# Kernel tuning notes

Hardware: AMD Instinct MI355X
Metric: run time of the kernel (lower is better)

The kernel has to match this reference:

```python
import jax, jax.numpy as jnp
import numpy as np
from jax import lax

B, N = 16, 131072
NUM_CLASSES = 2
OUTPUT_BOX_NUM = 500
IOU_THRESHOLD = 0.3
SCORE_THRESHOLD = 0.7
NEG = jnp.float32(-1e30)
DELTA_SCALE = jnp.array([0.1, 0.2], dtype=jnp.float32)


def setup_inputs() -> dict:
    key = jax.random.key(0)
    k1, k2, k3, k4, k5, k6 = jax.random.split(key, 6)
    deltas = jax.random.normal(k1, (B, N, 2), dtype=jnp.float32)
    class_logits = jax.random.normal(k2, (B, N, NUM_CLASSES), dtype=jnp.float32)
    # CTPN-style anchors: fixed-width 16px columns, varying y-center / height
    cy = jax.random.uniform(k3, (B, N), dtype=jnp.float32) * 1024.0
    h = 8.0 + jax.random.uniform(k4, (B, N), dtype=jnp.float32) * 56.0
    col = jax.random.randint(k5, (B, N), 0, 64).astype(jnp.float32) * 16.0
    anchors = jnp.stack([cy - 0.5 * h, col, cy + 0.5 * h, col + 16.0], axis=-1)  # [B,N,4] (y1,x1,y2,x2)
    valid_anchors_indices = jax.random.randint(k6, (B, N), 0, N)
    return {
        'deltas': deltas,
        'class_logits': class_logits,
        'anchors': anchors,
        'valid_anchors_indices': valid_anchors_indices,
    }


def apply_regress(deltas, anchors):
    # deltas [N,2] (dy,dh); anchors [N,4] (y1,x1,y2,x2)
    h = anchors[:, 2] - anchors[:, 0]
    cy = (anchors[:, 2] + anchors[:, 0]) * 0.5
    d = deltas * DELTA_SCALE
    cy = cy + d[:, 0] * h
    h = h * jnp.exp(d[:, 1])
    return jnp.stack([cy - 0.5 * h, anchors[:, 1], cy + 0.5 * h, anchors[:, 3]], axis=1)


def iou_one_to_many(box, boxes):
    yy1 = jnp.maximum(box[0], boxes[:, 0])
    xx1 = jnp.maximum(box[1], boxes[:, 1])
    yy2 = jnp.minimum(box[2], boxes[:, 2])
    xx2 = jnp.minimum(box[3], boxes[:, 3])
    inter = jnp.maximum(yy2 - yy1, 0.0) * jnp.maximum(xx2 - xx1, 0.0)
    a1 = (box[2] - box[0]) * (box[3] - box[1])
    a2 = (boxes[:, 2] - boxes[:, 0]) * (boxes[:, 3] - boxes[:, 1])
    return inter / (a1 + a2 - inter + 1e-8)


def nms_indices(boxes, scores):
    # Greedy NMS, fixed OUTPUT_BOX_NUM iterations (jit-compatible).
    active = jnp.where(scores >= SCORE_THRESHOLD, scores, NEG)

    def step(active, _):
        idx = jnp.argmax(active)
        valid = active[idx] > NEG
        iou = iou_one_to_many(boxes[idx], boxes)
        active = jnp.where(valid & (iou > IOU_THRESHOLD), NEG, active)
        return active, (idx, valid)

    _, (idxs, valids) = lax.scan(step, active, None, length=OUTPUT_BOX_NUM)
    return idxs, valids


def _forward(deltas, class_logits, anchors, valid_anchors_indices):
    # gather valid predictions per batch
    idx = valid_anchors_indices
    deltas_g = jnp.take_along_axis(deltas, idx[..., None], axis=1)          # [B,N,2]
    logits_g = jnp.take_along_axis(class_logits, idx[..., None], axis=1)    # [B,N,C]
    class_scores = jax.nn.softmax(logits_g, axis=-1)
    fg_scores = jnp.max(class_scores[..., 1:], axis=-1)                      # [B,N]
    proposals = jax.vmap(apply_regress)(deltas_g, anchors)                   # [B,N,4]

    def per_image(boxes, scores, logits):
        sel, valid = nms_indices(boxes, scores)
        m = valid.astype(boxes.dtype)[:, None]
        b = boxes[sel] * m                                                   # [K,4]
        s = scores[sel][:, None] * m                                         # [K,1]
        l = logits[sel] * m                                                  # [K,C]
        # pad_to_fixed_size appends a tag column (1 for real rows, 0 padding)
        return (jnp.concatenate([b, m], axis=1),
                jnp.concatenate([s, m], axis=1),
                jnp.concatenate([l, m], axis=1))

    return jax.vmap(per_image)(proposals, fg_scores, logits_g)


def reference(deltas, class_logits, anchors, valid_anchors_indices):
    return _forward(deltas, class_logits, anchors, valid_anchors_indices)
```

## Files before the change

kernel.cpp:

```cpp
#include <hip/hip_runtime.h>
#include <cstdint>

#define BATCH 16
#define NN 131072
#define NCOL 64
#define KOUT 500
#define GG 8
typedef unsigned long long u64;

__device__ __forceinline__ float fadd(float a, float b) { return __fadd_rn(a, b); }
__device__ __forceinline__ float fsub(float a, float b) { return __fsub_rn(a, b); }
__device__ __forceinline__ float fmul(float a, float b) { return __fmul_rn(a, b); }

__device__ __forceinline__ void regress(float ya, float yb, float dl0, float dl1,
                                        float& ny1, float& ny2) {
    float h  = fsub(yb, ya);
    float cy = fmul(fadd(yb, ya), 0.5f);
    float d0 = fmul(dl0, 0.1f);
    float d1 = fmul(dl1, 0.2f);
    cy = fadd(cy, fmul(d0, h));
    h  = fmul(h, expf(d1));
    ny1 = fsub(cy, fmul(0.5f, h));
    ny2 = fadd(cy, fmul(0.5f, h));
}

__device__ __forceinline__ float fg_score(float l0, float l1) {
    float mx = fmaxf(l0, l1);
    float e0 = expf(fsub(l0, mx));
    float e1 = expf(fsub(l1, mx));
    return e1 / fadd(e0, e1);
}

__device__ __forceinline__ u64 wave_max_u64(u64 v) {
#if __has_builtin(__builtin_amdgcn_update_dpp)
    unsigned hi = (unsigned)(v >> 32), lo = (unsigned)(v & 0xffffffffull);
#define DPP_STEP(C)                                                                     \
    {                                                                                   \
        unsigned ohi = (unsigned)__builtin_amdgcn_update_dpp((int)hi, (int)hi, C, 0xf, 0xf, false); \
        unsigned olo = (unsigned)__builtin_amdgcn_update_dpp((int)lo, (int)lo, C, 0xf, 0xf, false); \
        if (ohi > hi || (ohi == hi && olo > lo)) { hi = ohi; lo = olo; }                \
    }
    DPP_STEP(0x111)
    DPP_STEP(0x112)
    DPP_STEP(0x114)
    DPP_STEP(0x118)
    DPP_STEP(0x142)
    DPP_STEP(0x143)
#undef DPP_STEP
    u64 m = ((u64)hi << 32) | lo;
    return __shfl(m, 63);
#else
    for (int o = 32; o; o >>= 1) {
        u64 x = __shfl_xor(v, o);
        if (x > v) v = x;
    }
    return v;
#endif
}

__global__ __launch_bounds__(256, 4) void k_filter(const float* __restrict__ deltas,
                                                   const float* __restrict__ logits,
                                                   const float* __restrict__ anchors,
                                                   const int* __restrict__ vai,
                                                   int* __restrict__ cand_count,
                                                   float4* __restrict__ cand,
                                                   int cap) {
    __shared__ int lcnt[NCOL];
    __shared__ int gbase[NCOL];
    int j = blockIdx.x;
    int x = j & 7;
    int r = j >> 3;
    int b = 2 * x + (r >> 6);
    int c = r & 63;
    int base = b * NN + c * 2048;
    int tid = threadIdx.x;
    if (tid < NCOL) lcnt[tid] = 0;
    __syncthreads();

    int g[GG];
#pragma unroll
    for (int k = 0; k < GG; ++k) g[k] = vai[base + tid + (k << 8)];
    float4 an[GG];
#pragma unroll
    for (int k = 0; k < GG; ++k) an[k] = ((const float4*)anchors)[base + tid + (k << 8)];
    float2 lg[GG], dl[GG];
#pragma unroll
    for (int k = 0; k < GG; ++k) {
        size_t p = ((size_t)b * NN + g[k]) * 2;
        lg[k] = *(const float2*)(logits + p);
        dl[k] = *(const float2*)(deltas + p);
    }

    float sv[GG], y1v[GG], y2v[GG];
    int colv[GG], lpos[GG];
#pragma unroll
    for (int k = 0; k < GG; ++k) {
        float s = fg_score(lg[k].x, lg[k].y);
        lpos[k] = -1;
        if (s >= 0.7f) {
            regress(an[k].x, an[k].z, dl[k].x, dl[k].y, y1v[k], y2v[k]);
            sv[k] = s;
            int col = (int)(an[k].y * 0.0625f);
            colv[k] = col;
            lpos[k] = atomicAdd(&lcnt[col], 1);
        }
    }
    __syncthreads();
    if (tid < NCOL) gbase[tid] = atomicAdd(&cand_count[b * NCOL + tid], lcnt[tid]);
    __syncthreads();
#pragma unroll
    for (int k = 0; k < GG; ++k) {
        if (lpos[k] >= 0) {
            int col = colv[k];
            int pos = gbase[col] + lpos[k];
            int i = (base + tid + (k << 8)) & (NN - 1);
            if (pos < cap)
                cand[(size_t)(b * NCOL + col) * cap + pos] =
                    make_float4(sv[k], y1v[k], y2v[k], __int_as_float(i));
        }
    }
}

__global__ __launch_bounds__(64, 1) void k_nms(const int* __restrict__ cand_count,
                                               const float4* __restrict__ cand,
                                               u64* __restrict__ surv,
                                               int* __restrict__ surv_count,
                                               int cap) {
    __shared__ float sy1[1024], sy2[1024];
    int bc = blockIdx.x;
    int lane = threadIdx.x;
    int cnt = cand_count[bc];
    if (cnt > cap) cnt = cap;
    if (cnt > 1024) cnt = 1024;

    u64 kreg[16];
    float y1r[16], y2r[16];
#pragma unroll
    for (int k = 0; k < 16; ++k) {
        int jj = lane + (k << 6);
        u64 kk = 0ull;
        float a = 0.0f, bb = 0.0f;
        if (jj < cnt) {
            float4 cd = cand[(size_t)bc * cap + jj];
            int idx = __float_as_int(cd.w);
            kk = ((u64)__float_as_uint(cd.x) << 32) |
                 ((unsigned)(NN - 1 - idx) << 10) | (unsigned)jj;
            a = cd.y;
            bb = cd.z;
        }
        kreg[k] = kk; y1r[k] = a; y2r[k] = bb;
        sy1[jj] = a; sy2[jj] = bb;
    }
    u64 best = 0ull;
#pragma unroll
    for (int k = 0; k < 16; ++k)
        if (kreg[k] > best) best = kreg[k];
    best = wave_max_u64(best);

    u64* so = surv + (size_t)bc * KOUT;
    int ns = 0;
    while (best != 0ull) {
        if (lane == 0) so[ns] = best;
        ns++;
        if (ns == KOUT) break;
        int js = (int)(best & 1023ull);
        float ya = sy1[js], yb = sy2[js];
        float a1 = fmul(fsub(yb, ya), 16.0f);
        u64 nb = 0ull;
#pragma unroll
        for (int k = 0; k < 16; ++k) {
            if ((k << 6) < cnt) {
                u64 v = kreg[k];
                if (__any(v != 0ull)) {
                    float yy1 = fmaxf(ya, y1r[k]);
                    float yy2 = fminf(yb, y2r[k]);
                    float inter = fmul(fmaxf(fsub(yy2, yy1), 0.0f), 16.0f);
                    float a2 = fmul(fsub(y2r[k], y1r[k]), 16.0f);
                    float den = fadd(fsub(fadd(a1, a2), inter), 1e-8f);
                    float iou = inter / den;
                    if (v != 0ull) {
                        if (iou > 0.3f) kreg[k] = 0ull;
                        else if (v > nb) nb = v;
                    }
                }
            }
        }
        best = wave_max_u64(nb);
    }
    if (lane == 0) surv_count[bc] = ns;
}

__device__ __forceinline__ void merge_path(const u64* __restrict__ A, int nA,
                                           const u64* __restrict__ B, int nB,
                                           u64* __restrict__ O, int lane, int nt) {
    int L = nA + nB;
    if (L > KOUT) L = KOUT;
    for (int k = lane; k < L; k += nt) {
        int lo = k - nB; if (lo < 0) lo = 0;
        int hi = k < nA ? k : nA;
        while (lo < hi) {
            int mid = (lo + hi) >> 1;
            if (A[mid] > B[k - mid - 1]) lo = mid + 1;
            else hi = mid;
        }
        int i = lo, jj = k - lo;
        O[k] = (i < nA && (jj >= nB || A[i] > B[jj])) ? A[i] : B[jj];
    }
}

__global__ __launch_bounds__(256) void k_mtree(const u64* __restrict__ in,
                                               const int* __restrict__ incnt,
                                               u64* __restrict__ outb,
                                               int* __restrict__ outcnt) {
    __shared__ u64 L[8][512];
    __shared__ u64 P[4][512];
    int tid = threadIdx.x;
    int base = blockIdx.x * 8;
    auto nL = [&](int i) { int n = incnt[base + i]; return n > KOUT ? KOUT : n; };
    auto nP = [&](int i) { int n = nL(2 * i) + nL(2 * i + 1); return n > KOUT ? KOUT : n; };
    auto nQ = [&](int i) { int n = nP(2 * i) + nP(2 * i + 1); return n > KOUT ? KOUT : n; };
#pragma unroll
    for (int i = 0; i < 8; ++i) {
        int n = nL(i);
        const u64* p = in + (size_t)(base + i) * KOUT;
        for (int j = tid; j < n; j += 256) L[i][j] = p[j];
    }
    __syncthreads();
    {
        int g = tid >> 6, lane = tid & 63;
        merge_path(L[2 * g], nL(2 * g), L[2 * g + 1], nL(2 * g + 1), P[g], lane, 64);
    }
    __syncthreads();
    {
        int h = tid >> 7, lane = tid & 127;
        merge_path(P[2 * h], nP(2 * h), P[2 * h + 1], nP(2 * h + 1), L[h], lane, 128);
    }
    __syncthreads();
    merge_path(L[0], nQ(0), L[1], nQ(1), outb + (size_t)blockIdx.x * KOUT, tid, 256);
    if (tid == 0) {
        int n = nQ(0) + nQ(1);
        outcnt[blockIdx.x] = n > KOUT ? KOUT : n;
    }
}

__global__ void k_out(const u64* __restrict__ finalk,
                      const int* __restrict__ cntF,
                      const float* __restrict__ deltas,
                      const float* __restrict__ logits,
                      const float* __restrict__ anchors,
                      const int* __restrict__ vai,
                      float* __restrict__ out) {
    int t = blockIdx.x * blockDim.x + threadIdx.x;
    if (t >= BATCH * KOUT) return;
    int b = t / KOUT;
    int r = t % KOUT;
    int cnt = cntF[b];
    float y1 = 0, x1 = 0, y2 = 0, x2 = 0, s = 0, l0o = 0, l1o = 0, msk = 0;
    if (r < cnt) {
        u64 key = finalk[(size_t)b * KOUT + r];
        int i = NN - 1 - (int)((key >> 10) & 0x1FFFFull);
        int g = vai[(size_t)b * NN + i];
        size_t lbase = ((size_t)b * NN + g) * 2;
        float l0 = logits[lbase], l1 = logits[lbase + 1];
        s = fg_score(l0, l1);
        const float* an = anchors + ((size_t)b * NN + i) * 4;
        x1 = an[1];
        x2 = an[3];
        regress(an[0], an[2], deltas[lbase], deltas[lbase + 1], y1, y2);
        l0o = l0; l1o = l1; msk = 1.0f;
    }
    float* bo = out + (size_t)t * 5;
    bo[0] = y1; bo[1] = x1; bo[2] = y2; bo[3] = x2; bo[4] = msk;
    float* so = out + BATCH * KOUT * 5 + (size_t)t * 2;
    so[0] = s; so[1] = msk;
    float* lo = out + BATCH * KOUT * 7 + (size_t)t * 3;
    lo[0] = l0o; lo[1] = l1o; lo[2] = msk;
}

extern "C" void kernel_launch(void* const* d_in, const int* in_sizes, int n_in,
                              void* d_out, int out_size, void* d_ws, size_t ws_size,
                              hipStream_t stream) {
    const float* deltas  = (const float*)d_in[0];
    const float* logits  = (const float*)d_in[1];
    const float* anchors = (const float*)d_in[2];
    const int*   vai     = (const int*)d_in[3];
    float* out = (float*)d_out;

    int cap = 1024;
    auto need = [&](int c) -> size_t {
        size_t o = (size_t)BATCH * NCOL * 4 * 3;
        o = (o + 15) & ~(size_t)15;
        o += (size_t)BATCH * NCOL * c * 16;
        o += (size_t)BATCH * NCOL * KOUT * 8;
        return o;
    };
    while (cap > 256 && need(cap) > ws_size) cap >>= 1;

    char* ws = (char*)d_ws;
    size_t off = 0;
    int* cand_count = (int*)(ws + off); off += (size_t)BATCH * NCOL * 4;
    int* cntA       = (int*)(ws + off); off += (size_t)BATCH * NCOL * 4;
    int* cntB       = (int*)(ws + off); off += (size_t)BATCH * NCOL * 4;
    off = (off + 15) & ~(size_t)15;
    float4* cand = (float4*)(ws + off); off += (size_t)BATCH * NCOL * cap * 16;
    u64* surv = (u64*)(ws + off);
    u64* pong = (u64*)cand;

    hipMemsetAsync(cand_count, 0, (size_t)BATCH * NCOL * 4, stream);
    k_filter<<<1024, 256, 0, stream>>>(
        deltas, logits, anchors, vai, cand_count, cand, cap);
    k_nms<<<BATCH * NCOL, 64, 0, stream>>>(cand_count, cand, surv, cntA, cap);
    k_mtree<<<BATCH * 8, 256, 0, stream>>>(surv, cntA, pong, cntB);
    k_mtree<<<BATCH, 256, 0, stream>>>(pong, cntB, surv, cntA);
    k_out<<<(BATCH * KOUT + 255) / 256, 256, 0, stream>>>(
        surv, cntA, deltas, logits, anchors, vai, out);
}
```

Baseline: 336.3 us.

## Split per-column NMS into bounded first pass plus threshold-pruned resume pass

The per-column greedy NMS now runs only a limited number of iterations first. The partial survivors are merged to find the current 500th-best global key, and a second pass resumes NMS only in columns whose next candidate could still beat that threshold. Alive masks are saved in the first pass so the second pass can restore the column state. The winning box coordinates are also carried through the DPP argmax, so they no longer need to be read back from shared memory. This adds two extra merge-tree launches plus a resume kernel, and it needs more workspace. If the workspace is too small, the code falls back to the old single-pass path.

```diff
diff --git a/kernel.cpp b/kernel.cpp
--- a/kernel.cpp
+++ b/kernel.cpp
@@ -6,6 +6,7 @@
 #define NCOL 64
 #define KOUT 500
 #define GG 8
+#define ITERS_A 64
 typedef unsigned long long u64;
 
 __device__ __forceinline__ float fadd(float a, float b) { return __fadd_rn(a, b); }
@@ -31,31 +32,59 @@
     return e1 / fadd(e0, e1);
 }
 
-__device__ __forceinline__ u64 wave_max_u64(u64 v) {
+__device__ __forceinline__ void wave_argmax_box(u64& key, float& y1, float& y2) {
 #if __has_builtin(__builtin_amdgcn_update_dpp)
-    unsigned hi = (unsigned)(v >> 32), lo = (unsigned)(v & 0xffffffffull);
-#define DPP_STEP(C)                                                                     \
+    unsigned hi = (unsigned)(key >> 32), lo = (unsigned)(key & 0xffffffffull);
+    int a = __float_as_int(y1), b = __float_as_int(y2);
+#define STEP(C)                                                                         \
     {                                                                                   \
         unsigned ohi = (unsigned)__builtin_amdgcn_update_dpp((int)hi, (int)hi, C, 0xf, 0xf, false); \
         unsigned olo = (unsigned)__builtin_amdgcn_update_dpp((int)lo, (int)lo, C, 0xf, 0xf, false); \
-        if (ohi > hi || (ohi == hi && olo > lo)) { hi = ohi; lo = olo; }                \
-    }
-    DPP_STEP(0x111)
-    DPP_STEP(0x112)
-    DPP_STEP(0x114)
-    DPP_STEP(0x118)
-    DPP_STEP(0x142)
-    DPP_STEP(0x143)
-#undef DPP_STEP
-    u64 m = ((u64)hi << 32) | lo;
-    return __shfl(m, 63);
+        int oa = __builtin_amdgcn_update_dpp(a, a, C, 0xf, 0xf, false);                 \
+        int ob = __builtin_amdgcn_update_dpp(b, b, C, 0xf, 0xf, false);                 \
+        if (ohi > hi || (ohi == hi && olo > lo)) { hi = ohi; lo = olo; a = oa; b = ob; } \
+    }
+    STEP(0x111) STEP(0x112) STEP(0x114) STEP(0x118) STEP(0x142) STEP(0x143)
+#undef STEP
+    key = __shfl((u64)(((u64)hi << 32) | lo), 63);
+    y1  = __shfl(__int_as_float(a), 63);
+    y2  = __shfl(__int_as_float(b), 63);
 #else
     for (int o = 32; o; o >>= 1) {
-        u64 x = __shfl_xor(v, o);
-        if (x > v) v = x;
-    }
-    return v;
+        u64 ok = __shfl_xor(key, o);
+        float o1 = __shfl_xor(y1, o), o2 = __shfl_xor(y2, o);
+        if (ok > key) { key = ok; y1 = o1; y2 = o2; }
+    }
 #endif
+}
+
+__device__ __forceinline__ void nms_sweep(u64 (&kreg)[16], const float (&y1r)[16],
+                                          const float (&y2r)[16], int cnt,
+                                          float ya, float yb,
+                                          u64& best, float& by1, float& by2) {
+    float a1 = fmul(fsub(yb, ya), 16.0f);
+    u64 pb = 0ull;
+    float p1 = 0.0f, p2 = 0.0f;
+#pragma unroll
+    for (int k = 0; k < 16; ++k) {
+        if ((k << 6) < cnt) {
+            u64 v = kreg[k];
+            if (__any(v != 0ull)) {
+                float yy1 = fmaxf(ya, y1r[k]);
+                float yy2 = fminf(yb, y2r[k]);
+                float inter = fmul(fmaxf(fsub(yy2, yy1), 0.0f), 16.0f);
+                float a2 = fmul(fsub(y2r[k], y1r[k]), 16.0f);
+                float den = fadd(fsub(fadd(a1, a2), inter), 1e-8f);
+                float iou = inter / den;
+                if (v != 0ull) {
+                    if (iou > 0.3f) kreg[k] = 0ull;
+                    else if (v > pb) { pb = v; p1 = y1r[k]; p2 = y2r[k]; }
+                }
+            }
+        }
+    }
+    best = pb; by1 = p1; by2 = p2;
+    wave_argmax_box(best, by1, by2);
 }
 
 __global__ __launch_bounds__(256, 4) void k_filter(const float* __restrict__ deltas,
@@ -121,12 +150,13 @@
     }
 }
 
-__global__ __launch_bounds__(64, 1) void k_nms(const int* __restrict__ cand_count,
-                                               const float4* __restrict__ cand,
-                                               u64* __restrict__ surv,
-                                               int* __restrict__ surv_count,
-                                               int cap) {
-    __shared__ float sy1[1024], sy2[1024];
+__global__ __launch_bounds__(64, 1) void k_nmsA(const int* __restrict__ cand_count,
+                                                const float4* __restrict__ cand,
+                                                u64* __restrict__ surv,
+                                                int* __restrict__ surv_count,
+                                                u64* __restrict__ aliveB,
+                                                u64* __restrict__ nextb,
+                                                int cap, int iters) {
     int bc = blockIdx.x;
     int lane = threadIdx.x;
     int cnt = cand_count[bc];
@@ -138,54 +168,91 @@
 #pragma unroll
     for (int k = 0; k < 16; ++k) {
         int jj = lane + (k << 6);
-        u64 kk = 0ull;
-        float a = 0.0f, bb = 0.0f;
+        u64 kk = 0ull; float a = 0.0f, bb = 0.0f;
         if (jj < cnt) {
             float4 cd = cand[(size_t)bc * cap + jj];
             int idx = __float_as_int(cd.w);
             kk = ((u64)__float_as_uint(cd.x) << 32) |
                  ((unsigned)(NN - 1 - idx) << 10) | (unsigned)jj;
-            a = cd.y;
-            bb = cd.z;
+            a = cd.y; bb = cd.z;
         }
         kreg[k] = kk; y1r[k] = a; y2r[k] = bb;
-        sy1[jj] = a; sy2[jj] = bb;
-    }
-    u64 best = 0ull;
+    }
+    u64 best = 0ull; float ya = 0.0f, yb = 0.0f;
 #pragma unroll
     for (int k = 0; k < 16; ++k)
-        if (kreg[k] > best) best = kreg[k];
-    best = wave_max_u64(best);
+        if (kreg[k] > best) { best = kreg[k]; ya = y1r[k]; yb = y2r[k]; }
+    wave_argmax_box(best, ya, yb);
 
     u64* so = surv + (size_t)bc * KOUT;
     int ns = 0;
     while (best != 0ull) {
         if (lane == 0) so[ns] = best;
         ns++;
-        if (ns == KOUT) break;
-        int js = (int)(best & 1023ull);
-        float ya = sy1[js], yb = sy2[js];
-        float a1 = fmul(fsub(yb, ya), 16.0f);
-        u64 nb = 0ull;
+        if (ns >= KOUT) break;
+        nms_sweep(kreg, y1r, y2r, cnt, ya, yb, best, ya, yb);
+        if (ns >= iters) break;
+    }
+    if (lane == 0) surv_count[bc] = ns;
+    if (aliveB != nullptr) {
+        if (lane == 0) nextb[bc] = best;
 #pragma unroll
         for (int k = 0; k < 16; ++k) {
-            if ((k << 6) < cnt) {
-                u64 v = kreg[k];
-                if (__any(v != 0ull)) {
-                    float yy1 = fmaxf(ya, y1r[k]);
-                    float yy2 = fminf(yb, y2r[k]);
-                    float inter = fmul(fmaxf(fsub(yy2, yy1), 0.0f), 16.0f);
-                    float a2 = fmul(fsub(y2r[k], y1r[k]), 16.0f);
-                    float den = fadd(fsub(fadd(a1, a2), inter), 1e-8f);
-                    float iou = inter / den;
-                    if (v != 0ull) {
-                        if (iou > 0.3f) kreg[k] = 0ull;
-                        else if (v > nb) nb = v;
-                    }
-                }
-            }
-        }
-        best = wave_max_u64(nb);
+            u64 m = __ballot(kreg[k] != 0ull);
+            if (lane == 0) aliveB[(size_t)bc * 16 + k] = m;
+        }
+    }
+}
+
+__global__ __launch_bounds__(64, 1) void k_nmsB(const int* __restrict__ cand_count,
+                                                const float4* __restrict__ cand,
+                                                const u64* __restrict__ aliveB,
+                                                const u64* __restrict__ nextb,
+                                                u64* __restrict__ surv,
+                                                int* __restrict__ surv_count,
+                                                const u64* __restrict__ finalk,
+                                                const int* __restrict__ cntF,
+                                                int cap) {
+    int bc = blockIdx.x;
+    int lane = threadIdx.x;
+    int ns = surv_count[bc];
+    if (ns >= KOUT) return;
+    int b = bc >> 6;
+    u64 L = (cntF[b] >= KOUT) ? finalk[(size_t)b * KOUT + (KOUT - 1)] : 0ull;
+    u64 nb0 = nextb[bc];
+    if (nb0 == 0ull || nb0 < L) return;
+
+    int cnt = cand_count[bc];
+    if (cnt > cap) cnt = cap;
+    if (cnt > 1024) cnt = 1024;
+    u64 kreg[16];
+    float y1r[16], y2r[16];
+#pragma unroll
+    for (int k = 0; k < 16; ++k) {
+        int jj = lane + (k << 6);
+        u64 kk = 0ull; float a = 0.0f, bb = 0.0f;
+        if (jj < cnt) {
+            float4 cd = cand[(size_t)bc * cap + jj];
+            int idx = __float_as_int(cd.w);
+            kk = ((u64)__float_as_uint(cd.x) << 32) |
+                 ((unsigned)(NN - 1 - idx) << 10) | (unsigned)jj;
+            a = cd.y; bb = cd.z;
+        }
+        if (!((aliveB[(size_t)bc * 16 + k] >> lane) & 1ull)) kk = 0ull;
+        kreg[k] = kk; y1r[k] = a; y2r[k] = bb;
+    }
+    u64 best = 0ull; float ya = 0.0f, yb = 0.0f;
+#pragma unroll
+    for (int k = 0; k < 16; ++k)
+        if (kreg[k] > best) { best = kreg[k]; ya = y1r[k]; yb = y2r[k]; }
+    wave_argmax_box(best, ya, yb);
+
+    u64* so = surv + (size_t)bc * KOUT;
+    while (best != 0ull && best >= L) {
+        if (lane == 0) so[ns] = best;
+        ns++;
+        if (ns >= KOUT) break;
+        nms_sweep(kreg, y1r, y2r, cnt, ya, yb, best, ya, yb);
     }
     if (lane == 0) surv_count[bc] = ns;
 }
@@ -286,32 +353,62 @@
     const int*   vai     = (const int*)d_in[3];
     float* out = (float*)d_out;
 
+    char* ws = (char*)d_ws;
     int cap = 1024;
-    auto need = [&](int c) -> size_t {
-        size_t o = (size_t)BATCH * NCOL * 4 * 3;
-        o = (o + 15) & ~(size_t)15;
-        o += (size_t)BATCH * NCOL * c * 16;
-        o += (size_t)BATCH * NCOL * KOUT * 8;
-        return o;
-    };
-    while (cap > 256 && need(cap) > ws_size) cap >>= 1;
-
-    char* ws = (char*)d_ws;
+
     size_t off = 0;
-    int* cand_count = (int*)(ws + off); off += (size_t)BATCH * NCOL * 4;
-    int* cntA       = (int*)(ws + off); off += (size_t)BATCH * NCOL * 4;
-    int* cntB       = (int*)(ws + off); off += (size_t)BATCH * NCOL * 4;
-    off = (off + 15) & ~(size_t)15;
-    float4* cand = (float4*)(ws + off); off += (size_t)BATCH * NCOL * cap * 16;
-    u64* surv = (u64*)(ws + off);
-    u64* pong = (u64*)cand;
-
-    hipMemsetAsync(cand_count, 0, (size_t)BATCH * NCOL * 4, stream);
-    k_filter<<<1024, 256, 0, stream>>>(
-        deltas, logits, anchors, vai, cand_count, cand, cap);
-    k_nms<<<BATCH * NCOL, 64, 0, stream>>>(cand_count, cand, surv, cntA, cap);
-    k_mtree<<<BATCH * 8, 256, 0, stream>>>(surv, cntA, pong, cntB);
-    k_mtree<<<BATCH, 256, 0, stream>>>(pong, cntB, surv, cntA);
-    k_out<<<(BATCH * KOUT + 255) / 256, 256, 0, stream>>>(
-        surv, cntA, deltas, logits, anchors, vai, out);
-}
+    auto alloc = [&](size_t bytes) { void* p = ws + off; off += (bytes + 15) & ~(size_t)15; return p; };
+    int* cand_count = (int*)alloc(BATCH * NCOL * 4);
+    int* cntA       = (int*)alloc(BATCH * NCOL * 4);
+    int* cntM       = (int*)alloc(512 * 4);
+    int* cntF       = (int*)alloc(64);
+    u64* nextb      = (u64*)alloc(BATCH * NCOL * 8);
+    u64* alive      = (u64*)alloc((size_t)BATCH * NCOL * 16 * 8);
+    float4* cand    = (float4*)alloc((size_t)BATCH * NCOL * cap * 16);
+    u64* surv       = (u64*)alloc((size_t)BATCH * NCOL * KOUT * 8);
+    u64* pong       = (u64*)alloc((size_t)BATCH * 8 * KOUT * 8);
+    u64* finalb     = (u64*)alloc((size_t)BATCH * KOUT * 8);
+    bool full = (off <= ws_size);
+
+    if (full) {
+        hipMemsetAsync(cand_count, 0, (size_t)BATCH * NCOL * 4, stream);
+        k_filter<<<1024, 256, 0, stream>>>(deltas, logits, anchors, vai,
+                                           cand_count, cand, cap);
+        k_nmsA<<<BATCH * NCOL, 64, 0, stream>>>(cand_count, cand, surv, cntA,
+                                                alive, nextb, cap, ITERS_A);
+        k_mtree<<<BATCH * 8, 256, 0, stream>>>(surv, cntA, pong, cntM);
+        k_mtree<<<BATCH, 256, 0, stream>>>(pong, cntM, finalb, cntF);
+        k_nmsB<<<BATCH * NCOL, 64, 0, stream>>>(cand_count, cand, alive, nextb,
+                                                surv, cntA, finalb, cntF, cap);
+        k_mtree<<<BATCH * 8, 256, 0, stream>>>(surv, cntA, pong, cntM);
+        k_mtree<<<BATCH, 256, 0, stream>>>(pong, cntM, finalb, cntF);
+        k_out<<<(BATCH * KOUT + 255) / 256, 256, 0, stream>>>(
+            finalb, cntF, deltas, logits, anchors, vai, out);
+    } else {
+        auto need = [&](int c) -> size_t {
+            size_t o = (size_t)BATCH * NCOL * 4 * 2 + 512 * 4;
+            o = (o + 15) & ~(size_t)15;
+            o += (size_t)BATCH * NCOL * c * 16;
+            o += (size_t)BATCH * NCOL * KOUT * 8;
+            return o;
+        };
+        while (cap > 256 && need(cap) > ws_size) cap >>= 1;
+        off = 0;
+        cand_count = (int*)alloc(BATCH * NCOL * 4);
+        cntA       = (int*)alloc(BATCH * NCOL * 4);
+        cntM       = (int*)alloc(512 * 4);
+        cand       = (float4*)alloc((size_t)BATCH * NCOL * cap * 16);
+        surv       = (u64*)alloc((size_t)BATCH * NCOL * KOUT * 8);
+        pong       = (u64*)cand;
+
+        hipMemsetAsync(cand_count, 0, (size_t)BATCH * NCOL * 4, stream);
+        k_filter<<<1024, 256, 0, stream>>>(deltas, logits, anchors, vai,
+                                           cand_count, cand, cap);
+        k_nmsA<<<BATCH * NCOL, 64, 0, stream>>>(cand_count, cand, surv, cntA,
+                                                (u64*)nullptr, (u64*)nullptr, cap, KOUT);
+        k_mtree<<<BATCH * 8, 256, 0, stream>>>(surv, cntA, pong, cntM);
+        k_mtree<<<BATCH, 256, 0, stream>>>(pong, cntM, surv, cntA);
+        k_out<<<(BATCH * KOUT + 255) / 256, 256, 0, stream>>>(
+            surv, cntA, deltas, logits, anchors, vai, out);
+    }
+}
```

New measurement: 334.8 us. About the same (-0.4%).
